# Kernel optimization log

Hardware: AMD Instinct MI355X
Metric: run time of the kernel (lower is better)

The kernel has to match this reference:

```python
import jax, jax.numpy as jnp
import numpy as np

B, S, H = 1, 2048, 2048
NH, HD, RD = 32, 64, 64      # n_heads, head_dim, qk_mqa_dim (rope dim)
QR, KVR = 1024, 896          # q_lora_rank, kv_lora_rank
EPS = 1e-6
SCALE = HD ** -0.5           # scaling = head_dim ** -0.5 (as in module)


def rotate_half(x):
    x1, x2 = jnp.split(x, 2, axis=-1)
    return jnp.concatenate((-x2, x1), axis=-1)


def rmsnorm(x, w):
    var = jnp.mean(jnp.square(x), axis=-1, keepdims=True)
    return x * jax.lax.rsqrt(var + EPS) * w


def setup_inputs() -> dict:
    key = jax.random.key(0)
    ks = jax.random.split(key, 8)
    hidden_states = jax.random.normal(ks[0], (B, S, H), jnp.float32)
    # rotary tables over RD dims (applied only to the rope slice)
    inv_freq = 1.0 / (10000.0 ** (np.arange(0, RD, 2, dtype=np.float32) / RD))
    ang = np.arange(S, dtype=np.float32)[:, None] * inv_freq[None, :]
    emb = np.concatenate([ang, ang], axis=-1)  # [S, RD]
    cos = jnp.tile(jnp.asarray(np.cos(emb))[None], (B, 1, 1))
    sin = jnp.tile(jnp.asarray(np.sin(emb))[None], (B, 1, 1))
    s = 0.02
    q_a_w = s * jax.random.normal(ks[1], (QR, H), jnp.float32)
    q_a_ln_w = jnp.ones((QR,), jnp.float32)
    q_b_w = s * jax.random.normal(ks[2], (NH * (HD + RD), QR), jnp.float32)
    kv_a_w = s * jax.random.normal(ks[3], (KVR + RD, H), jnp.float32)
    kv_a_ln_w = jnp.ones((KVR,), jnp.float32)
    kv_b_w = s * jax.random.normal(ks[4], (NH * 2 * HD, KVR), jnp.float32)
    o_w = s * jax.random.normal(ks[5], (H, NH * HD), jnp.float32)
    return {"hidden_states": hidden_states, "cos": cos, "sin": sin,
            "q_a_w": q_a_w, "q_a_ln_w": q_a_ln_w, "q_b_w": q_b_w,
            "kv_a_w": kv_a_w, "kv_a_ln_w": kv_a_ln_w, "kv_b_w": kv_b_w,
            "o_w": o_w}


def reference(hidden_states, cos, sin, q_a_w, q_a_ln_w, q_b_w,
              kv_a_w, kv_a_ln_w, kv_b_w, o_w):
    b, s, _ = hidden_states.shape
    # Q: low-rank down -> RMSNorm -> up, split nope/rope per head
    q_lat = rmsnorm(hidden_states @ q_a_w.T, q_a_ln_w)             # [B,S,QR]
    q = (q_lat @ q_b_w.T).reshape(b, s, NH, HD + RD).transpose(0, 2, 1, 3)
    q_nope, q_rope = q[..., :HD], q[..., HD:]                      # [B,NH,S,HD/RD]
    # KV: joint down-proj with shared MQA rope key
    ckv = hidden_states @ kv_a_w.T                                 # [B,S,KVR+RD]
    c_kv, k_rope = ckv[..., :KVR], ckv[..., KVR:]
    k_rope = k_rope[:, None]                                       # [B,1,S,RD]
    kv = (rmsnorm(c_kv, kv_a_ln_w) @ kv_b_w.T).reshape(b, s, NH, 2 * HD)
    kv = kv.transpose(0, 2, 1, 3)                                  # [B,NH,S,2HD]
    k_nope, v = kv[..., :HD], kv[..., HD:]
    # RoPE on rope slices only (cos/sin unsqueezed over head dim)
    c_, s_ = cos[:, None], sin[:, None]
    q_rope = q_rope * c_ + rotate_half(q_rope) * s_
    k_rope = k_rope * c_ + rotate_half(k_rope) * s_
    q_full = jnp.concatenate([q_nope, q_rope], axis=-1)            # [B,NH,S,HD+RD]
    k_full = jnp.concatenate(
        [k_nope, jnp.broadcast_to(k_rope, (b, NH, s, RD))], axis=-1)
    # causal SDPA
    scores = jnp.einsum('bhqd,bhkd->bhqk', q_full, k_full) * SCALE
    mask = jnp.tril(jnp.ones((s, s), bool))
    scores = jnp.where(mask, scores, jnp.finfo(scores.dtype).min)
    attn = jax.nn.softmax(scores, axis=-1)
    out = jnp.einsum('bhqk,bhkd->bhqd', attn, v)                   # [B,NH,S,HD]
    out = out.transpose(0, 2, 1, 3).reshape(b, s, NH * HD)
    return out @ o_w.T                                             # [B,S,H]
```

## Files before the change

### kernel.cpp

```cpp
#include <hip/hip_runtime.h>


typedef __attribute__((ext_vector_type(8))) __bf16 bf16x8;
typedef __attribute__((ext_vector_type(4))) float f32x4;

__device__ __forceinline__ unsigned short f2bf(float f) {
  unsigned int x = __builtin_bit_cast(unsigned int, f);
  x += 0x7fffu + ((x >> 16) & 1u);
  return (unsigned short)(x >> 16);
}
__device__ __forceinline__ void gload_lds16(const void* g, void* l) {
  __builtin_amdgcn_global_load_lds(
      (const __attribute__((address_space(1))) void*)g,
      (__attribute__((address_space(3))) void*)l, 16, 0, 0);
}

struct CvtSegs {
  const float* src[6];
  unsigned short* dst[6];
  unsigned int n_src[6];
  unsigned int n_tot[6];
  unsigned int blk0[7];
};

__global__ __launch_bounds__(256) void cvt_all(CvtSegs sg) {
  int b = blockIdx.x;
  int seg = 0;
#pragma unroll
  for (int k = 0; k < 5; ++k)
    if (b >= (int)sg.blk0[k + 1]) seg = k + 1;
  size_t i = ((size_t)(b - sg.blk0[seg]) * 256 + threadIdx.x) * 4;
  if (i >= sg.n_tot[seg]) return;
  unsigned short o0 = 0, o1 = 0, o2 = 0, o3 = 0;
  if (i < sg.n_src[seg]) {
    float4 v = *reinterpret_cast<const float4*>(sg.src[seg] + i);
    o0 = f2bf(v.x); o1 = f2bf(v.y); o2 = f2bf(v.z); o3 = f2bf(v.w);
  }
  *reinterpret_cast<ushort4*>(sg.dst[seg] + i) = make_ushort4(o0, o1, o2, o3);
}

__global__ __launch_bounds__(512, 4) void gemm_bt2(const unsigned short* __restrict__ A,
                                                   const unsigned short* __restrict__ B,
                                                   float* __restrict__ C,
                                                   int M, int N, int K) {
  __shared__ unsigned short lA0[128 * 64], lA1[128 * 64];
  __shared__ unsigned short lB0[64 * 64], lB1[64 * 64];
  const int tid = threadIdx.x, lane = tid & 63, wv = tid >> 6;
  const int wr = wv >> 1, wc = wv & 1;
  const int bm = blockIdx.y * 128, bn = blockIdx.x * 64;

  f32x4 acc[2][2] = {};

  const int ar0 = tid >> 3;
  const int acol = (tid & 7) * 8;

  auto stage = [&](unsigned short* la, unsigned short* lb, int k0) {
#pragma unroll
    for (int i = 0; i < 2; ++i)
      gload_lds16(A + (size_t)(bm + i * 64 + ar0) * K + k0 + acol,
                  &la[(i * 512 + wv * 64) * 8]);
    gload_lds16(B + (size_t)(bn + ar0) * K + k0 + acol, &lb[(wv * 64) * 8]);
  };

  auto compute = [&](const unsigned short* la, const unsigned short* lb) {
#pragma unroll
    for (int ks = 0; ks < 2; ++ks) {
      bf16x8 af[2], bfr[2];
#pragma unroll
      for (int m = 0; m < 2; ++m)
        af[m] = *reinterpret_cast<const bf16x8*>(
            &la[(wr * 32 + m * 16 + (lane & 15)) * 64 + ks * 32 + (lane >> 4) * 8]);
#pragma unroll
      for (int n = 0; n < 2; ++n)
        bfr[n] = *reinterpret_cast<const bf16x8*>(
            &lb[(wc * 32 + n * 16 + (lane & 15)) * 64 + ks * 32 + (lane >> 4) * 8]);
      __builtin_amdgcn_s_setprio(1);
#pragma unroll
      for (int m = 0; m < 2; ++m)
#pragma unroll
        for (int n = 0; n < 2; ++n)
          acc[m][n] = __builtin_amdgcn_mfma_f32_16x16x32_bf16(af[m], bfr[n], acc[m][n], 0, 0, 0);
      __builtin_amdgcn_s_setprio(0);
    }
  };

  stage(lA0, lB0, 0);
  for (int k0 = 0; k0 < K; k0 += 128) {
    __syncthreads();
    stage(lA1, lB1, k0 + 64);
    compute(lA0, lB0);
    __syncthreads();
    if (k0 + 128 < K) stage(lA0, lB0, k0 + 128);
    compute(lA1, lB1);
  }

  const int r0 = bm + wr * 32, c0 = bn + wc * 32;
#pragma unroll
  for (int m = 0; m < 2; ++m)
#pragma unroll
    for (int n = 0; n < 2; ++n)
#pragma unroll
      for (int r = 0; r < 4; ++r)
        C[(size_t)(r0 + m * 16 + (lane >> 4) * 4 + r) * N + c0 + n * 16 + (lane & 15)] =
            acc[m][n][r];
}

__global__ __launch_bounds__(256) void rmsnorm_rope(const float* __restrict__ C1,
                                                    const float* __restrict__ qw,
                                                    const float* __restrict__ kvw,
                                                    const float* __restrict__ cosp,
                                                    const float* __restrict__ sinp,
                                                    unsigned short* __restrict__ qn,
                                                    unsigned short* __restrict__ ckvn,
                                                    unsigned short* __restrict__ kr) {
  const int s = blockIdx.x, tid = threadIdx.x;
  const float* row = C1 + (size_t)s * 2048;
  __shared__ float red[4];

  float4 v = *reinterpret_cast<const float4*>(row + tid * 4);
  float ss = v.x * v.x + v.y * v.y + v.z * v.z + v.w * v.w;
  ss += __shfl_xor(ss, 32); ss += __shfl_xor(ss, 16); ss += __shfl_xor(ss, 8);
  ss += __shfl_xor(ss, 4);  ss += __shfl_xor(ss, 2);  ss += __shfl_xor(ss, 1);
  if ((tid & 63) == 0) red[tid >> 6] = ss;
  __syncthreads();
  float rs = rsqrtf((red[0] + red[1] + red[2] + red[3]) * (1.f / 1024.f) + 1e-6f);
  {
    float4 w = *reinterpret_cast<const float4*>(qw + tid * 4);
    *reinterpret_cast<ushort4*>(qn + (size_t)s * 1024 + tid * 4) =
        make_ushort4(f2bf(v.x * rs * w.x), f2bf(v.y * rs * w.y),
                     f2bf(v.z * rs * w.z), f2bf(v.w * rs * w.w));
  }

  float4 u = make_float4(0.f, 0.f, 0.f, 0.f);
  if (tid < 224) u = *reinterpret_cast<const float4*>(row + 1024 + tid * 4);
  ss = u.x * u.x + u.y * u.y + u.z * u.z + u.w * u.w;
  ss += __shfl_xor(ss, 32); ss += __shfl_xor(ss, 16); ss += __shfl_xor(ss, 8);
  ss += __shfl_xor(ss, 4);  ss += __shfl_xor(ss, 2);  ss += __shfl_xor(ss, 1);
  __syncthreads();
  if ((tid & 63) == 0) red[tid >> 6] = ss;
  __syncthreads();
  rs = rsqrtf((red[0] + red[1] + red[2] + red[3]) * (1.f / 896.f) + 1e-6f);
  if (tid < 224) {
    float4 w = *reinterpret_cast<const float4*>(kvw + tid * 4);
    *reinterpret_cast<ushort4*>(ckvn + (size_t)s * 896 + tid * 4) =
        make_ushort4(f2bf(u.x * rs * w.x), f2bf(u.y * rs * w.y),
                     f2bf(u.z * rs * w.z), f2bf(u.w * rs * w.w));
  }

  if (tid < 64) {
    int d = tid;
    float x = row[1920 + d];
    float part = (d < 32) ? -row[1920 + d + 32] : row[1920 + d - 32];
    float vv = x * cosp[(size_t)s * 64 + d] + part * sinp[(size_t)s * 64 + d];
    kr[(size_t)s * 64 + d] = f2bf(vv);
  }
}

__global__ __launch_bounds__(256) void q_post(const float* __restrict__ Qf,
                                              const float* __restrict__ cosp,
                                              const float* __restrict__ sinp,
                                              unsigned short* __restrict__ Qb) {
  size_t base = ((size_t)blockIdx.x * 256 + threadIdx.x) * 4;
  int s = (int)(base >> 12);
  int w = (int)(base & 127);
  float4 x = *reinterpret_cast<const float4*>(Qf + base);
  float4 o;
  if (w < 64) {
    o = x;
  } else {
    int d = w - 64;
    float sgn = (d < 32) ? -1.f : 1.f;
    float4 prt = (d < 32) ? *reinterpret_cast<const float4*>(Qf + base + 32)
                          : *reinterpret_cast<const float4*>(Qf + base - 32);
    float4 c = *reinterpret_cast<const float4*>(cosp + (size_t)s * 64 + d);
    float4 sn = *reinterpret_cast<const float4*>(sinp + (size_t)s * 64 + d);
    o.x = x.x * c.x + sgn * prt.x * sn.x;
    o.y = x.y * c.y + sgn * prt.y * sn.y;
    o.z = x.z * c.z + sgn * prt.z * sn.z;
    o.w = x.w * c.w + sgn * prt.w * sn.w;
  }
  const float SC = 0.18033688f;
  *reinterpret_cast<ushort4*>(Qb + base) =
      make_ushort4(f2bf(o.x * SC), f2bf(o.y * SC), f2bf(o.z * SC), f2bf(o.w * SC));
}

__global__ __launch_bounds__(256) void kv_post(const float* __restrict__ KVf,
                                               const unsigned short* __restrict__ kr,
                                               unsigned short* __restrict__ Kb,
                                               unsigned short* __restrict__ Vt) {
  __shared__ float lT[64 * 65];
  const int s0 = blockIdx.x * 64, h = blockIdx.y, tid = threadIdx.x;
  for (int idx = tid; idx < 4096; idx += 256) {
    int r = idx >> 6, c = idx & 63;
    size_t base = (size_t)(s0 + r) * 4096 + h * 128;
    Kb[base + c] = f2bf(KVf[base + c]);
    Kb[base + 64 + c] = kr[(size_t)(s0 + r) * 64 + c];
    lT[r * 65 + c] = KVf[base + 64 + c];
  }
  __syncthreads();
  for (int idx = tid; idx < 4096; idx += 256) {
    int d = idx >> 6, c = idx & 63;
    Vt[((size_t)h * 64 + d) * 2048 + s0 + c] = f2bf(lT[c * 65 + d]);
  }
}

__global__ __launch_bounds__(256) void flash_attn(const unsigned short* __restrict__ Qb,
                                                  const unsigned short* __restrict__ Kb,
                                                  const unsigned short* __restrict__ Vt,
                                                  unsigned short* __restrict__ Ao) {
  __shared__ unsigned short lK0[64 * 128], lK1[64 * 128];
  __shared__ unsigned short lP[64 * 72];
  const int tid = threadIdx.x, lane = tid & 63, wv = tid >> 6;
  const int h = blockIdx.x;
  const int qb = (int)gridDim.y - 1 - (int)blockIdx.y;
  const int q0 = qb * 64;
  const int nt = qb + 1;
  const int firstrow = q0 + wv * 16;
  const int qa = firstrow + (lane & 15);

  bf16x8 qf[4];
  {
    const unsigned short* qrow = Qb + (size_t)(firstrow + (lane & 15)) * 4096 + h * 128;
#pragma unroll
    for (int ks = 0; ks < 4; ++ks)
      qf[ks] = *reinterpret_cast<const bf16x8*>(qrow + ks * 32 + (lane >> 4) * 8);
  }

  f32x4 o_acc[4] = {};
  float mrow = -1e30f, lrow = 0.f;

  const int krow = wv * 4 + (lane >> 4);
  const int kcol = (((lane & 15) ^ (krow & 7)) * 8);
  const int swz = lane & 7;

  auto stage = [&](int t, unsigned short* lK) {
    int j0 = t * 64;
#pragma unroll
    for (int i = 0; i < 4; ++i)
      gload_lds16(Kb + (size_t)(j0 + i * 16 + krow) * 4096 + h * 128 + kcol,
                  &lK[(i * 16 + wv * 4) * 128]);
  };

  auto loadV = [&](int j0, bf16x8 (&vr)[2][4]) {
#pragma unroll
    for (int ks = 0; ks < 2; ++ks)
#pragma unroll
      for (int n = 0; n < 4; ++n)
        vr[ks][n] = *reinterpret_cast<const bf16x8*>(
            Vt + ((size_t)h * 64 + n * 16 + (lane & 15)) * 2048 + j0 + ks * 32 +
            (lane >> 4) * 8);
  };

  auto computeT = [&](int j0, const unsigned short* lK, const bf16x8 (&vr)[2][4]) {
    f32x4 sT[4] = {};
    __builtin_amdgcn_s_setprio(1);
#pragma unroll
    for (int n = 0; n < 4; ++n)
#pragma unroll
      for (int ks = 0; ks < 4; ++ks) {
        bf16x8 kf = *reinterpret_cast<const bf16x8*>(
            &lK[(n * 16 + (lane & 15)) * 128 + (((ks * 4 + (lane >> 4)) ^ swz)) * 8]);
        sT[n] = __builtin_amdgcn_mfma_f32_16x16x32_bf16(kf, qf[ks], sT[n], 0, 0, 0);
      }
    __builtin_amdgcn_s_setprio(0);

    if (j0 == q0) {
#pragma unroll
      for (int n = 0; n < 4; ++n)
#pragma unroll
        for (int r = 0; r < 4; ++r) {
          int key = j0 + n * 16 + (lane >> 4) * 4 + r;
          if (key > qa) sT[n][r] = -1e30f;
        }
    }

    float mx = sT[0][0];
#pragma unroll
    for (int n = 0; n < 4; ++n)
#pragma unroll
      for (int r = 0; r < 4; ++r) mx = fmaxf(mx, sT[n][r]);
    mx = fmaxf(mx, __shfl_xor(mx, 16));
    mx = fmaxf(mx, __shfl_xor(mx, 32));

    if (__any(mx - mrow > 8.0f)) {
      float mn = fmaxf(mrow, mx);
      float sf = exp2f(mrow - mn);
      mrow = mn;
      lrow *= sf;
      float sfr[4];
#pragma unroll
      for (int r = 0; r < 4; ++r) sfr[r] = __shfl(sf, (lane >> 4) * 4 + r);
#pragma unroll
      for (int n = 0; n < 4; ++n)
#pragma unroll
        for (int r = 0; r < 4; ++r) o_acc[n][r] *= sfr[r];
    }

    float ps = 0.f;
#pragma unroll
    for (int n = 0; n < 4; ++n)
#pragma unroll
      for (int r = 0; r < 4; ++r) {
        float p = exp2f(sT[n][r] - mrow);
        ps += p;
        lP[(wv * 16 + (lane & 15)) * 72 + n * 16 + (lane >> 4) * 4 + r] = f2bf(p);
      }
    ps += __shfl_xor(ps, 16);
    ps += __shfl_xor(ps, 32);
    lrow += ps;

    __builtin_amdgcn_s_setprio(1);
#pragma unroll
    for (int ks = 0; ks < 2; ++ks) {
      bf16x8 pa = *reinterpret_cast<const bf16x8*>(
          &lP[(wv * 16 + (lane & 15)) * 72 + ks * 32 + (lane >> 4) * 8]);
#pragma unroll
      for (int n = 0; n < 4; ++n)
        o_acc[n] = __builtin_amdgcn_mfma_f32_16x16x32_bf16(pa, vr[ks][n], o_acc[n], 0, 0, 0);
    }
    __builtin_amdgcn_s_setprio(0);
  };

  bf16x8 vr0[2][4], vr1[2][4];
  stage(0, lK0);
  for (int t = 0; t < nt; t += 2) {
    loadV(t * 64, vr0);
    __syncthreads();
    if (t + 1 < nt) stage(t + 1, lK1);
    computeT(t * 64, lK0, vr0);
    if (t + 1 < nt) {
      loadV((t + 1) * 64, vr1);
      __syncthreads();
      if (t + 2 < nt) stage(t + 2, lK0);
      computeT((t + 1) * 64, lK1, vr1);
    }
  }

  float inv = 1.f / lrow;
  float invr[4];
#pragma unroll
  for (int r = 0; r < 4; ++r) invr[r] = __shfl(inv, (lane >> 4) * 4 + r);
#pragma unroll
  for (int n = 0; n < 4; ++n)
#pragma unroll
    for (int r = 0; r < 4; ++r) {
      float o = o_acc[n][r] * invr[r];
      Ao[(size_t)(firstrow + (lane >> 4) * 4 + r) * 2048 + h * 64 + n * 16 + (lane & 15)] =
          f2bf(o);
    }
}

extern "C" void kernel_launch(void* const* d_in, const int* in_sizes, int n_in,
                              void* d_out, int out_size, void* d_ws, size_t ws_size,
                              hipStream_t stream) {
  const float* hs   = (const float*)d_in[0];
  const float* cosp = (const float*)d_in[1];
  const float* sinp = (const float*)d_in[2];
  const float* qaw  = (const float*)d_in[3];
  const float* qaln = (const float*)d_in[4];
  const float* qbwf = (const float*)d_in[5];
  const float* kvaw = (const float*)d_in[6];
  const float* kvln = (const float*)d_in[7];
  const float* kvbwf= (const float*)d_in[8];
  const float* owf  = (const float*)d_in[9];
  float* out = (float*)d_out;
  char* ws = (char*)d_ws;
  const size_t MB = 1u << 20;

  unsigned short* W1b  = (unsigned short*)(ws + 0);
  unsigned short* Ao   = (unsigned short*)(ws + 0);
  unsigned short* qbw  = (unsigned short*)(ws + 8 * MB);
  unsigned short* Vt   = (unsigned short*)(ws + 8 * MB);
  unsigned short* kvbw = (unsigned short*)(ws + 16 * MB);
  unsigned short* owb  = (unsigned short*)(ws + 23 * MB);
  unsigned short* hsb  = (unsigned short*)(ws + 31 * MB);
  unsigned short* Qb   = (unsigned short*)(ws + 31 * MB);
  float*          C1   = (float*)(ws + 39 * MB);
  unsigned short* Kb   = (unsigned short*)(ws + 47 * MB);
  unsigned short* qln  = (unsigned short*)(ws + 55 * MB);
  unsigned short* ckvn = (unsigned short*)(ws + 59 * MB);
  unsigned short* kr   = (unsigned short*)(ws + 63 * MB);
  float*          Qf   = (float*)(ws + 64 * MB);
  float*          KVf  = (float*)(ws + 96 * MB);
  (void)ws_size; (void)in_sizes; (void)n_in; (void)out_size;

  CvtSegs sg;
  sg.src[0] = qaw;   sg.dst[0] = W1b;                      sg.n_src[0] = 1024u * 2048u; sg.n_tot[0] = 1024u * 2048u;
  sg.src[1] = kvaw;  sg.dst[1] = W1b + (size_t)1024 * 2048; sg.n_src[1] = 960u * 2048u;  sg.n_tot[1] = 1024u * 2048u;
  sg.src[2] = hs;    sg.dst[2] = hsb;                      sg.n_src[2] = 2048u * 2048u; sg.n_tot[2] = 2048u * 2048u;
  sg.src[3] = qbwf;  sg.dst[3] = qbw;                      sg.n_src[3] = 4096u * 1024u; sg.n_tot[3] = 4096u * 1024u;
  sg.src[4] = kvbwf; sg.dst[4] = kvbw;                     sg.n_src[4] = 4096u * 896u;  sg.n_tot[4] = 4096u * 896u;
  sg.src[5] = owf;   sg.dst[5] = owb;                      sg.n_src[5] = 2048u * 2048u; sg.n_tot[5] = 2048u * 2048u;
  sg.blk0[0] = 0;
  for (int k = 0; k < 6; ++k) sg.blk0[k + 1] = sg.blk0[k] + sg.n_tot[k] / 1024u;
  cvt_all<<<dim3(sg.blk0[6]), 256, 0, stream>>>(sg);

  gemm_bt2<<<dim3(32, 16), 512, 0, stream>>>(hsb, W1b, C1, 2048, 2048, 2048);
  rmsnorm_rope<<<2048, 256, 0, stream>>>(C1, qaln, kvln, cosp, sinp, qln, ckvn, kr);
  gemm_bt2<<<dim3(64, 16), 512, 0, stream>>>(qln, qbw, Qf, 2048, 4096, 1024);
  gemm_bt2<<<dim3(64, 16), 512, 0, stream>>>(ckvn, kvbw, KVf, 2048, 4096, 896);

  q_post<<<dim3((unsigned)(((size_t)2048 * 4096) / 1024)), 256, 0, stream>>>(Qf, cosp, sinp, Qb);
  kv_post<<<dim3(32, 32), 256, 0, stream>>>(KVf, kr, Kb, Vt);

  flash_attn<<<dim3(32, 32), 256, 0, stream>>>(Qb, Kb, Vt, Ao);

  gemm_bt2<<<dim3(32, 16), 512, 0, stream>>>(Ao, owb, out, 2048, 2048, 2048);
}
```

Measured before the change: 260.7 us.

## Swizzle GEMM LDS tiles and pass attention P via shuffles instead of LDS

Applies an XOR swizzle to the GEMM's LDS A/B tiles on both the global-to-LDS stage and the fragment reads, to reduce LDS bank conflicts. In flash attention, the P tile is no longer written to LDS and read back. Probabilities are packed into bf16 pairs with v_cvt_pk_bf16_f32 and rearranged into the MFMA A-operand layout with cross-lane shuffles. It also adds an occupancy hint of 4 blocks per SM to flash_attn. This removes an LDS round trip and its scalar stores, at the cost of 16 shuffles per tile and higher register pressure.

```diff
diff --git a/kernel.cpp b/kernel.cpp
--- a/kernel.cpp
+++ b/kernel.cpp
@@ -3,6 +3,7 @@
 
 typedef __attribute__((ext_vector_type(8))) __bf16 bf16x8;
 typedef __attribute__((ext_vector_type(4))) float f32x4;
+typedef __attribute__((ext_vector_type(4))) unsigned u32x4;
 
 __device__ __forceinline__ unsigned short f2bf(float f) {
   unsigned int x = __builtin_bit_cast(unsigned int, f);
@@ -52,7 +53,8 @@
   f32x4 acc[2][2] = {};
 
   const int ar0 = tid >> 3;
-  const int acol = (tid & 7) * 8;
+  const int acol = (((tid & 7) ^ ((tid >> 3) & 7))) * 8;
+  const int swz = lane & 7;
 
   auto stage = [&](unsigned short* la, unsigned short* lb, int k0) {
 #pragma unroll
@@ -65,15 +67,16 @@
   auto compute = [&](const unsigned short* la, const unsigned short* lb) {
 #pragma unroll
     for (int ks = 0; ks < 2; ++ks) {
+      const int ch = ((ks * 4 + (lane >> 4)) ^ swz) * 8;
       bf16x8 af[2], bfr[2];
 #pragma unroll
       for (int m = 0; m < 2; ++m)
         af[m] = *reinterpret_cast<const bf16x8*>(
-            &la[(wr * 32 + m * 16 + (lane & 15)) * 64 + ks * 32 + (lane >> 4) * 8]);
+            &la[(wr * 32 + m * 16 + (lane & 15)) * 64 + ch]);
 #pragma unroll
       for (int n = 0; n < 2; ++n)
         bfr[n] = *reinterpret_cast<const bf16x8*>(
-            &lb[(wc * 32 + n * 16 + (lane & 15)) * 64 + ks * 32 + (lane >> 4) * 8]);
+            &lb[(wc * 32 + n * 16 + (lane & 15)) * 64 + ch]);
       __builtin_amdgcn_s_setprio(1);
 #pragma unroll
       for (int m = 0; m < 2; ++m)
@@ -204,12 +207,11 @@
   }
 }
 
-__global__ __launch_bounds__(256) void flash_attn(const unsigned short* __restrict__ Qb,
-                                                  const unsigned short* __restrict__ Kb,
-                                                  const unsigned short* __restrict__ Vt,
-                                                  unsigned short* __restrict__ Ao) {
+__global__ __launch_bounds__(256, 4) void flash_attn(const unsigned short* __restrict__ Qb,
+                                                     const unsigned short* __restrict__ Kb,
+                                                     const unsigned short* __restrict__ Vt,
+                                                     unsigned short* __restrict__ Ao) {
   __shared__ unsigned short lK0[64 * 128], lK1[64 * 128];
-  __shared__ unsigned short lP[64 * 72];
   const int tid = threadIdx.x, lane = tid & 63, wv = tid >> 6;
   const int h = blockIdx.x;
   const int qb = (int)gridDim.y - 1 - (int)blockIdx.y;
@@ -229,6 +231,11 @@
   f32x4 o_acc[4] = {};
   float mrow = -1e30f, lrow = 0.f;
 
+  const int g = lane >> 4;
+  const int sl0 = ((g & 1) * 2) * 16 + (lane & 15);
+  const int sl1 = sl0 + 16;
+  const bool hi = g >= 2;
+
   const int krow = wv * 4 + (lane >> 4);
   const int kcol = (((lane & 15) ^ (krow & 7)) * 8);
   const int swz = lane & 7;
@@ -269,7 +276,7 @@
       for (int n = 0; n < 4; ++n)
 #pragma unroll
         for (int r = 0; r < 4; ++r) {
-          int key = j0 + n * 16 + (lane >> 4) * 4 + r;
+          int key = j0 + n * 16 + g * 4 + r;
           if (key > qa) sT[n][r] = -1e30f;
         }
     }
@@ -297,28 +304,39 @@
     }
 
     float ps = 0.f;
-#pragma unroll
-    for (int n = 0; n < 4; ++n)
-#pragma unroll
-      for (int r = 0; r < 4; ++r) {
-        float p = exp2f(sT[n][r] - mrow);
-        ps += p;
-        lP[(wv * 16 + (lane & 15)) * 72 + n * 16 + (lane >> 4) * 4 + r] = f2bf(p);
-      }
+    unsigned dw[4][2];
+#pragma unroll
+    for (int n = 0; n < 4; ++n) {
+      float p0 = exp2f(sT[n][0] - mrow), p1 = exp2f(sT[n][1] - mrow);
+      float p2 = exp2f(sT[n][2] - mrow), p3 = exp2f(sT[n][3] - mrow);
+      ps += (p0 + p1) + (p2 + p3);
+      asm("v_cvt_pk_bf16_f32 %0, %1, %2" : "=v"(dw[n][0]) : "v"(p0), "v"(p1));
+      asm("v_cvt_pk_bf16_f32 %0, %1, %2" : "=v"(dw[n][1]) : "v"(p2), "v"(p3));
+    }
     ps += __shfl_xor(ps, 16);
     ps += __shfl_xor(ps, 32);
     lrow += ps;
 
-    __builtin_amdgcn_s_setprio(1);
 #pragma unroll
     for (int ks = 0; ks < 2; ++ks) {
-      bf16x8 pa = *reinterpret_cast<const bf16x8*>(
-          &lP[(wv * 16 + (lane & 15)) * 72 + ks * 32 + (lane >> 4) * 8]);
+      unsigned A0 = __shfl(dw[2 * ks][0], sl0);
+      unsigned B0 = __shfl(dw[2 * ks + 1][0], sl0);
+      unsigned A1 = __shfl(dw[2 * ks][1], sl0);
+      unsigned B1 = __shfl(dw[2 * ks + 1][1], sl0);
+      unsigned A2 = __shfl(dw[2 * ks][0], sl1);
+      unsigned B2 = __shfl(dw[2 * ks + 1][0], sl1);
+      unsigned A3 = __shfl(dw[2 * ks][1], sl1);
+      unsigned B3 = __shfl(dw[2 * ks + 1][1], sl1);
+      u32x4 mm;
+      mm.x = hi ? B0 : A0; mm.y = hi ? B1 : A1;
+      mm.z = hi ? B2 : A2; mm.w = hi ? B3 : A3;
+      bf16x8 pa = __builtin_bit_cast(bf16x8, mm);
+      __builtin_amdgcn_s_setprio(1);
 #pragma unroll
       for (int n = 0; n < 4; ++n)
         o_acc[n] = __builtin_amdgcn_mfma_f32_16x16x32_bf16(pa, vr[ks][n], o_acc[n], 0, 0, 0);
-    }
-    __builtin_amdgcn_s_setprio(0);
+      __builtin_amdgcn_s_setprio(0);
+    }
   };
 
   bf16x8 vr0[2][4], vr1[2][4];
```

Result: faster. 224.6 us (-13.9%).
